# Kernel optimization log

Measured on AMD Instinct MI355X. Metric: run time of the kernel, lower is better.

## Reference

```python
import jax, jax.numpy as jnp
import numpy as np

N_COLS = 4096
N_ROWS = 4096
H = 64          # args.hidden1
S = 2           # per-edge supp feature count (cv_supp/vc_supp dim 0)
S_VO = 2        # vo_supp feature dim
S_CO = 2        # co_supp feature dim
EDGE_DENSITY = 0.03


def setup_inputs() -> dict:
    key = jax.random.key(0)
    ks = jax.random.split(key, 20)
    col_hidden = jax.random.normal(ks[0], (N_COLS, H), jnp.float32)
    row_hidden = jax.random.normal(ks[1], (N_ROWS, H), jnp.float32)
    obj_hidden = jax.random.normal(ks[2], (1, H), jnp.float32)
    # sparse bipartite adjacency encoded in supp[0] != 0 (as in the TF code)
    mask = jax.random.bernoulli(ks[3], EDGE_DENSITY, (N_ROWS, N_COLS))
    cv_supp = jax.random.normal(ks[4], (S, N_ROWS, N_COLS), jnp.float32) * mask[None]
    vc_supp = jnp.transpose(cv_supp, (0, 2, 1))  # [S, ncols, nrows]
    vo_supp = jax.random.normal(ks[5], (N_COLS, S_VO), jnp.float32)
    co_supp = jax.random.normal(ks[6], (N_ROWS, S_CO), jnp.float32)
    w = 0.05
    W_vo = jax.random.normal(ks[7], (2 * H, H), jnp.float32) * w
    W_oc = jax.random.normal(ks[8], (2 * H, H), jnp.float32) * w
    W_vc = jax.random.normal(ks[9], (2 * H, H), jnp.float32) * w
    W_co = jax.random.normal(ks[10], (2 * H, H), jnp.float32) * w
    W_ov = jax.random.normal(ks[11], (2 * H, H), jnp.float32) * w
    W_cv = jax.random.normal(ks[12], (2 * H, H), jnp.float32) * w
    # attention scorer nets: Dense(concat_dim -> 1) + sigmoid
    w_attn_vo = jax.random.normal(ks[13], (2 * H + S_VO, 1), jnp.float32) * 0.1
    b_attn_vo = jnp.zeros((), jnp.float32)
    w_attn_co = jax.random.normal(ks[14], (2 * H + S_CO, 1), jnp.float32) * 0.1
    b_attn_co = jnp.zeros((), jnp.float32)
    # pairwise attn nets decomposed into [col | supp | row] weight slices
    w_cv_col = jax.random.normal(ks[15], (H,), jnp.float32) * 0.1
    w_cv_supp = jax.random.normal(ks[16], (S,), jnp.float32) * 0.1
    w_cv_row = jax.random.normal(ks[17], (H,), jnp.float32) * 0.1
    b_cv = jnp.zeros((), jnp.float32)
    w_vc_row = jax.random.normal(ks[18], (H,), jnp.float32) * 0.1
    w_vc_supp = jax.random.normal(ks[19], (S,), jnp.float32) * 0.1
    w_vc_col = jax.random.normal(jax.random.fold_in(key, 99), (H,), jnp.float32) * 0.1
    b_vc = jnp.zeros((), jnp.float32)
    return dict(col_hidden=col_hidden, row_hidden=row_hidden, obj_hidden=obj_hidden,
                cv_supp=cv_supp, vc_supp=vc_supp, vo_supp=vo_supp, co_supp=co_supp,
                W_vo=W_vo, W_oc=W_oc, W_vc=W_vc, W_co=W_co, W_ov=W_ov, W_cv=W_cv,
                w_attn_vo=w_attn_vo, b_attn_vo=b_attn_vo,
                w_attn_co=w_attn_co, b_attn_co=b_attn_co,
                w_cv_col=w_cv_col, w_cv_supp=w_cv_supp, w_cv_row=w_cv_row, b_cv=b_cv,
                w_vc_row=w_vc_row, w_vc_supp=w_vc_supp, w_vc_col=w_vc_col, b_vc=b_vc)


def _forward(col_hidden, row_hidden, obj_hidden, cv_supp, vc_supp, vo_supp, co_supp,
             W_vo, W_oc, W_vc, W_co, W_ov, W_cv,
             w_attn_vo, b_attn_vo, w_attn_co, b_attn_co,
             w_cv_col, w_cv_supp, w_cv_row, b_cv,
             w_vc_row, w_vc_supp, w_vc_col, b_vc):
    act = jax.nn.relu
    ncols, nrows = col_hidden.shape[0], row_hidden.shape[0]
    # ---- v -> o: attend over all columns, update obj node ----
    vo_in = jnp.concatenate([col_hidden, vo_supp,
                             jnp.broadcast_to(obj_hidden, (ncols, H))], axis=1)
    a_vo = jax.nn.sigmoid(vo_in @ w_attn_vo + b_attn_vo)          # [ncols, 1]
    v_o_out = a_vo.T @ col_hidden                                  # [1, H]
    obj = act(jnp.concatenate([obj_hidden, v_o_out], axis=1) @ W_vo)
    # ---- v -> c: per-row ragged neighbor attention, vectorized via masked pairwise scores ----
    nbr_cv = cv_supp[0] != 0                                       # [nrows, ncols]
    logits_cv = ((row_hidden @ w_cv_row)[:, None]
                 + (col_hidden @ w_cv_col)[None, :]
                 + jnp.einsum('snc,s->nc', cv_supp, w_cv_supp) + b_cv)
    score_cv = jnp.where(nbr_cv, jax.nn.sigmoid(logits_cv), 0.0)   # [nrows, ncols]
    v_out = score_cv @ col_hidden                                  # [nrows, H]
    o_c_out = act(jnp.concatenate([jnp.broadcast_to(obj, (nrows, H)), row_hidden], axis=1) @ W_oc)
    row_next = act(jnp.concatenate([o_c_out, v_out], axis=1) @ W_vc)
    # ---- c -> o ----
    co_in = jnp.concatenate([row_next, co_supp,
                             jnp.broadcast_to(obj, (nrows, H))], axis=1)
    a_co = jax.nn.sigmoid(co_in @ w_attn_co + b_attn_co)           # [nrows, 1]
    c_o_out = a_co.T @ row_next                                    # [1, H]
    obj = act(jnp.concatenate([obj, c_o_out], axis=1) @ W_co)
    # ---- c -> v ----
    nbr_vc = vc_supp[0] != 0                                       # [ncols, nrows]
    logits_vc = ((col_hidden @ w_vc_col)[:, None]
                 + (row_next @ w_vc_row)[None, :]
                 + jnp.einsum('scn,s->cn', vc_supp, w_vc_supp) + b_vc)
    score_vc = jnp.where(nbr_vc, jax.nn.sigmoid(logits_vc), 0.0)   # [ncols, nrows]
    c_out = score_vc @ row_next                                    # [ncols, H]
    o_v_out = act(jnp.concatenate([jnp.broadcast_to(obj, (ncols, H)), col_hidden], axis=1) @ W_ov)
    col_next = act(jnp.concatenate([o_v_out, c_out], axis=1) @ W_cv)
    return col_next, row_next, obj


def reference(col_hidden, row_hidden, obj_hidden, cv_supp, vc_supp, vo_supp, co_supp,
              W_vo, W_oc, W_vc, W_co, W_ov, W_cv,
              w_attn_vo, b_attn_vo, w_attn_co, b_attn_co,
              w_cv_col, w_cv_supp, w_cv_row, b_cv,
              w_vc_row, w_vc_supp, w_vc_col, b_vc):
    col_next, row_next, obj = _forward(
        col_hidden, row_hidden, obj_hidden, cv_supp, vc_supp, vo_supp, co_supp,
        W_vo, W_oc, W_vc, W_co, W_ov, W_cv,
        w_attn_vo, b_attn_vo, w_attn_co, b_attn_co,
        w_cv_col, w_cv_supp, w_cv_row, b_cv,
        w_vc_row, w_vc_supp, w_vc_col, b_vc)
    # original layer also passes the supp tensors through unchanged
    return (col_next, row_next, obj, cv_supp, vc_supp, vo_supp, co_supp)
```

## Files before the change

### kernel.cpp

```cpp
#include <hip/hip_runtime.h>
#include <math.h>

typedef float f4  __attribute__((ext_vector_type(4)));
typedef short s8v __attribute__((ext_vector_type(8)));
typedef unsigned short u16;
typedef u16 us4 __attribute__((ext_vector_type(4)));

#define PLANE (4096*4096)

#define OUT_COL 0
#define OUT_ROW 262144
#define OUT_OBJ 524288
#define OUT_CV  524352
#define OUT_VC  34078784
#define OUT_VO  67633216
#define OUT_CO  67641408

#define WS_VO_P  0
#define WS_CO_P  1024
#define WS_OBJ1  2048
#define WS_RDCV  2112
#define WS_CDCV  6208
#define WS_RDVC  10304
#define WS_CDVC  14400
#define WS_GPART 18496
#define WS_SC    2115648
#define WS_BT1   10504256
#define WS_BT2   10635328

__device__ __forceinline__ float sigf(float x) {
    return 1.0f / (1.0f + __expf(-x));
}
__device__ __forceinline__ u16 f2bf(float x) {
    unsigned u = __float_as_uint(x);
    return (u16)((u + 0x7FFFu + ((u >> 16) & 1u)) >> 16);
}

__device__ __forceinline__ void transpose_tile(int k0, int t,
    const float* __restrict__ X, u16* __restrict__ BT, float* lds )
{
    #pragma unroll
    for (int it = 0; it < 4; ++it) {
        const int idx = it * 256 + t;
        const int r = idx >> 4, c4 = (idx & 15) * 4;
        f4 v = *(const f4*)(X + (size_t)(k0 + r) * 64 + c4);
        *(f4*)(lds + r * 72 + c4) = v;
    }
    __syncthreads();
    #pragma unroll
    for (int it = 0; it < 4; ++it) {
        const int idx = it * 256 + t;
        const int h = idx >> 4, q = (idx & 15) * 4;
        us4 o;
        o.x = f2bf(lds[(q + 0) * 72 + h]);
        o.y = f2bf(lds[(q + 1) * 72 + h]);
        o.z = f2bf(lds[(q + 2) * 72 + h]);
        o.w = f2bf(lds[(q + 3) * 72 + h]);
        *(us4*)(BT + (size_t)h * 4096 + k0 + q) = o;
    }
}

__device__ __forceinline__ void attn_body(
    int blk, int t, const float* __restrict__ X, const float* __restrict__ supp,
    const float* __restrict__ obj, const float* __restrict__ wat,
    const float* __restrict__ bat, float* __restrict__ accP,
    float* sA, float* sAcc)
{
    const int i = blk * 256 + t;
    float od = 0.f;
    for (int h = 0; h < 64; ++h) od += obj[h] * wat[66 + h];
    float x = bat[0] + od + supp[i*2] * wat[64] + supp[i*2+1] * wat[65];
    const f4* Xr = (const f4*)(X + i*64);
    f4 xd = 0.f;
    #pragma unroll
    for (int q = 0; q < 16; ++q) xd += Xr[q] * ((const f4*)wat)[q];
    x += xd.x + xd.y + xd.z + xd.w;
    sA[t] = sigf(x);
    if (t < 64) sAcc[t] = 0.f;
    __syncthreads();
    const int w = t >> 6, h = t & 63;
    const int base = blk * 256 + w * 64;
    float partial = 0.f;
    for (int j = 0; j < 64; ++j)
        partial += sA[w*64 + j] * X[(base + j)*64 + h];
    atomicAdd(&sAcc[h], partial);
    __syncthreads();
    if (t < 64) accP[blk*64 + t] = sAcc[t];
}

__global__ __launch_bounds__(256) void k_front(
    const float* __restrict__ col_hidden, const float* __restrict__ row_hidden,
    const float* __restrict__ w_cv_col, const float* __restrict__ w_vc_col,
    const float* __restrict__ w_cv_row,
    float* __restrict__ cdcv, float* __restrict__ cdvc, float* __restrict__ rdcv,
    const float* __restrict__ vo_supp, const float* __restrict__ co_supp,
    float* __restrict__ out_vo, float* __restrict__ out_co,
    const float* __restrict__ obj_hidden, const float* __restrict__ w_attn_vo,
    const float* __restrict__ b_attn_vo, float* __restrict__ voP,
    u16* __restrict__ BT1)
{
    __shared__ float sA[256];
    __shared__ float sAcc[64];
    __shared__ float tr[64*72];
    const int t = threadIdx.x;
    if (blockIdx.x < 3072) {
        const int gw = blockIdx.x * 4 + (t >> 6);
        const int lane = t & 63;
        const int which = gw >> 12;
        const int row = gw & 4095;
        const float* x; const float* w; float* dst;
        if (which == 0)      { x = col_hidden; w = w_cv_col; dst = cdcv; }
        else if (which == 1) { x = col_hidden; w = w_vc_col; dst = cdvc; }
        else                 { x = row_hidden; w = w_cv_row; dst = rdcv; }
        float v = x[row * 64 + lane] * w[lane];
        #pragma unroll
        for (int off = 32; off; off >>= 1) v += __shfl_down(v, off, 64);
        if (lane == 0) dst[row] = v;
        return;
    }
    if (blockIdx.x < 3088) {
        const int idx = (blockIdx.x - 3072) * 256 + t;
        if (idx < 2048) ((f4*)out_vo)[idx] = ((const f4*)vo_supp)[idx];
        else            ((f4*)out_co)[idx - 2048] = ((const f4*)co_supp)[idx - 2048];
        return;
    }
    if (blockIdx.x < 3104) {
        attn_body(blockIdx.x - 3088, t, col_hidden, vo_supp, obj_hidden,
                  w_attn_vo, b_attn_vo, voP, sA, sAcc);
        return;
    }
    transpose_tile((blockIdx.x - 3104) * 64, t, col_hidden, BT1, tr);
}

__global__ __launch_bounds__(256) void k_attn(
    const float* __restrict__ X, const float* __restrict__ supp,
    const float* __restrict__ obj, const float* __restrict__ wat,
    const float* __restrict__ bat, float* __restrict__ accP,
    u16* __restrict__ BT2)
{
    __shared__ float sA[256];
    __shared__ float sAcc[64];
    __shared__ float tr[64*72];
    if (blockIdx.x < 16) {
        attn_body(blockIdx.x, threadIdx.x, X, supp, obj, wat, bat, accP, sA, sAcc);
        return;
    }
    transpose_tile((blockIdx.x - 16) * 64, threadIdx.x, X, BT2, tr);
}

__global__ __launch_bounds__(256) void k_copy(
    const float* __restrict__ a, const float* __restrict__ b,
    float* __restrict__ da, float* __restrict__ db)
{
    const int t = threadIdx.x;
    const f4* src; f4* dst; size_t off;
    if (blockIdx.x < 8192) { src = (const f4*)a; dst = (f4*)da; off = (size_t)blockIdx.x * 1024; }
    else                   { src = (const f4*)b; dst = (f4*)db; off = (size_t)(blockIdx.x - 8192) * 1024; }
    #pragma unroll
    for (int it = 0; it < 4; ++it) {
        const size_t i = off + t + it * 256;
        dst[i] = src[i];
    }
}

__global__ __launch_bounds__(256) void k_score(
    const float* __restrict__ supp0, const float* __restrict__ supp1,
    const float* __restrict__ perrow, const float* __restrict__ percol,
    const float* __restrict__ wsup, const float* __restrict__ bias,
    u16* __restrict__ score)
{
    const float w0 = wsup[0], w1 = wsup[1], bv = bias[0];
    const float rd = perrow[blockIdx.x];
    const size_t base = (size_t)blockIdx.x * 1024 + threadIdx.x;
    #pragma unroll
    for (int it = 0; it < 4; ++it) {
        const size_t idx = base + it * 256;
        const int j0 = (int)(idx & 1023) * 4;
        f4 a0 = ((const f4*)supp0)[idx];
        f4 a1 = ((const f4*)supp1)[idx];
        f4 cd = *(const f4*)(percol + j0);
        f4 lg = rd + cd + w0 * a0 + w1 * a1 + bv;
        us4 o;
        o.x = (a0.x != 0.f) ? f2bf(sigf(lg.x)) : (u16)0;
        o.y = (a0.y != 0.f) ? f2bf(sigf(lg.y)) : (u16)0;
        o.z = (a0.z != 0.f) ? f2bf(sigf(lg.z)) : (u16)0;
        o.w = (a0.w != 0.f) ? f2bf(sigf(lg.w)) : (u16)0;
        ((us4*)score)[idx] = o;
    }
}

__global__ __launch_bounds__(256, 4) void k_gemm(
    const u16* __restrict__ sc, const u16* __restrict__ BT,
    float* __restrict__ part,
    const float* __restrict__ objL, const float* __restrict__ objRp,
    const float* __restrict__ Wobj, float* __restrict__ objDst)
{
    __shared__ float rsum[64];
    const int t = threadIdx.x;
    if (blockIdx.x == 512) {
        if (t < 64) {
            float r = 0.f;
            for (int b = 0; b < 16; ++b) r += objRp[b*64 + t];
            rsum[t] = r;
        }
        __syncthreads();
        if (t < 64) {
            float acc = 0.f;
            for (int k = 0; k < 64; ++k) acc += objL[k] * Wobj[k*64 + t];
            for (int k = 0; k < 64; ++k) acc += rsum[k] * Wobj[(64+k)*64 + t];
            objDst[t] = fmaxf(acc, 0.f);
        }
        return;
    }
    const int mblk = blockIdx.x >> 3;
    const int ks   = blockIdx.x & 7;
    const int wv   = t >> 6, lane = t & 63;
    const int i0   = mblk * 64 + wv * 16;
    const int m    = lane & 15, quad = lane >> 4;
    const int k0   = ks * 512;

    f4 acc0 = 0.f, acc1 = 0.f, acc2 = 0.f, acc3 = 0.f;
    const u16* ap  = sc + (size_t)(i0 + m) * 4096 + k0 + quad * 8;
    const u16* bp  = BT + (size_t)m * 4096 + k0 + quad * 8;
    #pragma unroll 4
    for (int kc = 0; kc < 512; kc += 32) {
        s8v a  = *(const s8v*)(ap + kc);
        s8v b0 = *(const s8v*)(bp + kc);
        s8v b1 = *(const s8v*)(bp + 16 * 4096 + kc);
        s8v b2 = *(const s8v*)(bp + 32 * 4096 + kc);
        s8v b3 = *(const s8v*)(bp + 48 * 4096 + kc);
        acc0 = __builtin_amdgcn_mfma_f32_16x16x32_bf16(a, b0, acc0, 0, 0, 0);
        acc1 = __builtin_amdgcn_mfma_f32_16x16x32_bf16(a, b1, acc1, 0, 0, 0);
        acc2 = __builtin_amdgcn_mfma_f32_16x16x32_bf16(a, b2, acc2, 0, 0, 0);
        acc3 = __builtin_amdgcn_mfma_f32_16x16x32_bf16(a, b3, acc3, 0, 0, 0);
    }
    float* pb = part + (size_t)ks * 262144;
    #pragma unroll
    for (int r = 0; r < 4; ++r) {
        const size_t ro = (size_t)(i0 + quad * 4 + r) * 64 + m;
        pb[ro +  0] = acc0[r];
        pb[ro + 16] = acc1[r];
        pb[ro + 32] = acc2[r];
        pb[ro + 48] = acc3[r];
    }
}

__global__ __launch_bounds__(256) void k_mlp2(
    const float* __restrict__ objx, const float* __restrict__ base,
    const float* __restrict__ W1, const float* __restrict__ part,
    const float* __restrict__ W2, float* __restrict__ dst,
    const float* __restrict__ wvcrow, float* __restrict__ rdvc)
{
    __shared__ float mid[4][64];
    __shared__ float accs[4][64];
    const int t = threadIdx.x, w = t >> 6, h = t & 63;
    const int n = blockIdx.x * 4 + w;
    float v = 0.f;
    #pragma unroll
    for (int j = 0; j < 8; ++j) v += part[(size_t)j * 262144 + n*64 + h];
    accs[w][h] = v;
    float m = 0.f;
    for (int k = 0; k < 64; ++k) m += objx[k] * W1[k*64 + h];
    for (int k = 0; k < 64; ++k) m += base[n*64 + k] * W1[(64+k)*64 + h];
    mid[w][h] = fmaxf(m, 0.f);
    __syncthreads();
    float o = 0.f;
    for (int k = 0; k < 64; ++k) o += mid[w][k] * W2[k*64 + h];
    for (int k = 0; k < 64; ++k) o += accs[w][k] * W2[(64+k)*64 + h];
    o = fmaxf(o, 0.f);
    dst[n*64 + h] = o;
    if (rdvc) {
        float rv = o * wvcrow[h];
        #pragma unroll
        for (int off = 32; off; off >>= 1) rv += __shfl_down(rv, off, 64);
        if (h == 0) rdvc[n] = rv;
    }
}

extern "C" void kernel_launch(void* const* d_in, const int* in_sizes, int n_in,
                              void* d_out, int out_size, void* d_ws, size_t ws_size,
                              hipStream_t stream)
{
    const float* col_hidden = (const float*)d_in[0];
    const float* row_hidden = (const float*)d_in[1];
    const float* obj_hidden = (const float*)d_in[2];
    const float* cv_supp    = (const float*)d_in[3];
    const float* vc_supp    = (const float*)d_in[4];
    const float* vo_supp    = (const float*)d_in[5];
    const float* co_supp    = (const float*)d_in[6];
    const float* W_vo       = (const float*)d_in[7];
    const float* W_oc       = (const float*)d_in[8];
    const float* W_vc       = (const float*)d_in[9];
    const float* W_co       = (const float*)d_in[10];
    const float* W_ov       = (const float*)d_in[11];
    const float* W_cv       = (const float*)d_in[12];
    const float* w_attn_vo  = (const float*)d_in[13];
    const float* b_attn_vo  = (const float*)d_in[14];
    const float* w_attn_co  = (const float*)d_in[15];
    const float* b_attn_co  = (const float*)d_in[16];
    const float* w_cv_col   = (const float*)d_in[17];
    const float* w_cv_supp  = (const float*)d_in[18];
    const float* w_cv_row   = (const float*)d_in[19];
    const float* b_cv       = (const float*)d_in[20];
    const float* w_vc_row   = (const float*)d_in[21];
    const float* w_vc_supp  = (const float*)d_in[22];
    const float* w_vc_col   = (const float*)d_in[23];
    const float* b_vc       = (const float*)d_in[24];

    float* out = (float*)d_out;
    float* ws  = (float*)d_ws;
    u16* SC  = (u16*)(ws + WS_SC);
    u16* BT1 = (u16*)(ws + WS_BT1);
    u16* BT2 = (u16*)(ws + WS_BT2);

    k_front<<<3168, 256, 0, stream>>>(col_hidden, row_hidden, w_cv_col, w_vc_col, w_cv_row,
                                      ws + WS_CDCV, ws + WS_CDVC, ws + WS_RDCV,
                                      vo_supp, co_supp, out + OUT_VO, out + OUT_CO,
                                      obj_hidden, w_attn_vo, b_attn_vo, ws + WS_VO_P, BT1);
    k_copy<<<16384, 256, 0, stream>>>(cv_supp, vc_supp, out + OUT_CV, out + OUT_VC);
    k_score<<<4096, 256, 0, stream>>>(cv_supp, cv_supp + PLANE,
                                      ws + WS_RDCV, ws + WS_CDCV, w_cv_supp, b_cv, SC);
    k_gemm<<<513, 256, 0, stream>>>(SC, BT1, ws + WS_GPART,
                                    obj_hidden, ws + WS_VO_P, W_vo, ws + WS_OBJ1);
    k_mlp2<<<1024, 256, 0, stream>>>(ws + WS_OBJ1, row_hidden, W_oc, ws + WS_GPART, W_vc,
                                     out + OUT_ROW, w_vc_row, ws + WS_RDVC);
    k_attn<<<80, 256, 0, stream>>>(out + OUT_ROW, co_supp, ws + WS_OBJ1, w_attn_co,
                                   b_attn_co, ws + WS_CO_P, BT2);
    k_score<<<4096, 256, 0, stream>>>(vc_supp, vc_supp + PLANE,
                                      ws + WS_CDVC, ws + WS_RDVC, w_vc_supp, b_vc, SC);
    k_gemm<<<513, 256, 0, stream>>>(SC, BT2, ws + WS_GPART,
                                    ws + WS_OBJ1, ws + WS_CO_P, W_co, out + OUT_OBJ);
    k_mlp2<<<1024, 256, 0, stream>>>(out + OUT_OBJ, col_hidden, W_ov, ws + WS_GPART, W_cv,
                                     out + OUT_COL, nullptr, nullptr);
}
```

Baseline: 647.1 us.

## Fuse score computation and supp passthrough copy into the bf16 MFMA GEMM

Result: faster. 578.5 us (-10.6%).

```diff
diff --git a/kernel.cpp b/kernel.cpp
--- a/kernel.cpp
+++ b/kernel.cpp
@@ -24,9 +24,8 @@
 #define WS_RDVC  10304
 #define WS_CDVC  14400
 #define WS_GPART 18496
-#define WS_SC    2115648
-#define WS_BT1   10504256
-#define WS_BT2   10635328
+#define WS_BT1   4212800
+#define WS_BT2   4343872
 
 __device__ __forceinline__ float sigf(float x) {
     return 1.0f / (1.0f + __expf(-x));
@@ -148,56 +147,19 @@
     transpose_tile((blockIdx.x - 16) * 64, threadIdx.x, X, BT2, tr);
 }
 
-__global__ __launch_bounds__(256) void k_copy(
-    const float* __restrict__ a, const float* __restrict__ b,
-    float* __restrict__ da, float* __restrict__ db)
-{
-    const int t = threadIdx.x;
-    const f4* src; f4* dst; size_t off;
-    if (blockIdx.x < 8192) { src = (const f4*)a; dst = (f4*)da; off = (size_t)blockIdx.x * 1024; }
-    else                   { src = (const f4*)b; dst = (f4*)db; off = (size_t)(blockIdx.x - 8192) * 1024; }
-    #pragma unroll
-    for (int it = 0; it < 4; ++it) {
-        const size_t i = off + t + it * 256;
-        dst[i] = src[i];
-    }
-}
-
-__global__ __launch_bounds__(256) void k_score(
+__global__ __launch_bounds__(256, 4) void k_fgemm(
     const float* __restrict__ supp0, const float* __restrict__ supp1,
-    const float* __restrict__ perrow, const float* __restrict__ percol,
+    const u16* __restrict__ BT,
+    const float* __restrict__ rdot, const float* __restrict__ cdot,
     const float* __restrict__ wsup, const float* __restrict__ bias,
-    u16* __restrict__ score)
-{
-    const float w0 = wsup[0], w1 = wsup[1], bv = bias[0];
-    const float rd = perrow[blockIdx.x];
-    const size_t base = (size_t)blockIdx.x * 1024 + threadIdx.x;
-    #pragma unroll
-    for (int it = 0; it < 4; ++it) {
-        const size_t idx = base + it * 256;
-        const int j0 = (int)(idx & 1023) * 4;
-        f4 a0 = ((const f4*)supp0)[idx];
-        f4 a1 = ((const f4*)supp1)[idx];
-        f4 cd = *(const f4*)(percol + j0);
-        f4 lg = rd + cd + w0 * a0 + w1 * a1 + bv;
-        us4 o;
-        o.x = (a0.x != 0.f) ? f2bf(sigf(lg.x)) : (u16)0;
-        o.y = (a0.y != 0.f) ? f2bf(sigf(lg.y)) : (u16)0;
-        o.z = (a0.z != 0.f) ? f2bf(sigf(lg.z)) : (u16)0;
-        o.w = (a0.w != 0.f) ? f2bf(sigf(lg.w)) : (u16)0;
-        ((us4*)score)[idx] = o;
-    }
-}
-
-__global__ __launch_bounds__(256, 4) void k_gemm(
-    const u16* __restrict__ sc, const u16* __restrict__ BT,
+    float* __restrict__ pass0, float* __restrict__ pass1,
     float* __restrict__ part,
     const float* __restrict__ objL, const float* __restrict__ objRp,
     const float* __restrict__ Wobj, float* __restrict__ objDst)
 {
     __shared__ float rsum[64];
     const int t = threadIdx.x;
-    if (blockIdx.x == 512) {
+    if (blockIdx.x == 1024) {
         if (t < 64) {
             float r = 0.f;
             for (int b = 0; b < 16; ++b) r += objRp[b*64 + t];
@@ -212,19 +174,42 @@
         }
         return;
     }
-    const int mblk = blockIdx.x >> 3;
-    const int ks   = blockIdx.x & 7;
+    const int mblk = blockIdx.x >> 4;
+    const int ks   = blockIdx.x & 15;
     const int wv   = t >> 6, lane = t & 63;
     const int i0   = mblk * 64 + wv * 16;
     const int m    = lane & 15, quad = lane >> 4;
-    const int k0   = ks * 512;
+    const int k0   = ks * 256;
+    const float rd = rdot[i0 + m];
+    const float w0 = wsup[0], w1 = wsup[1], bv = bias[0];
 
     f4 acc0 = 0.f, acc1 = 0.f, acc2 = 0.f, acc3 = 0.f;
-    const u16* ap  = sc + (size_t)(i0 + m) * 4096 + k0 + quad * 8;
-    const u16* bp  = BT + (size_t)m * 4096 + k0 + quad * 8;
-    #pragma unroll 4
-    for (int kc = 0; kc < 512; kc += 32) {
-        s8v a  = *(const s8v*)(ap + kc);
+    const size_t arow = (size_t)(i0 + m) * 4096 + k0 + quad * 8;
+    const u16* bp = BT + (size_t)m * 4096 + k0 + quad * 8;
+
+    for (int kc = 0; kc < 256; kc += 32) {
+        f4 a0l = *(const f4*)(supp0 + arow + kc);
+        f4 a0h = *(const f4*)(supp0 + arow + kc + 4);
+        f4 a1l = *(const f4*)(supp1 + arow + kc);
+        f4 a1h = *(const f4*)(supp1 + arow + kc + 4);
+        *(f4*)(pass0 + arow + kc)     = a0l;
+        *(f4*)(pass0 + arow + kc + 4) = a0h;
+        *(f4*)(pass1 + arow + kc)     = a1l;
+        *(f4*)(pass1 + arow + kc + 4) = a1h;
+        const int kabs = k0 + quad * 8 + kc;
+        f4 cdl = *(const f4*)(cdot + kabs);
+        f4 cdh = *(const f4*)(cdot + kabs + 4);
+        f4 lgl = rd + cdl + w0 * a0l + w1 * a1l + bv;
+        f4 lgh = rd + cdh + w0 * a0h + w1 * a1h + bv;
+        s8v a;
+        a[0] = (short)((a0l.x != 0.f) ? f2bf(sigf(lgl.x)) : (u16)0);
+        a[1] = (short)((a0l.y != 0.f) ? f2bf(sigf(lgl.y)) : (u16)0);
+        a[2] = (short)((a0l.z != 0.f) ? f2bf(sigf(lgl.z)) : (u16)0);
+        a[3] = (short)((a0l.w != 0.f) ? f2bf(sigf(lgl.w)) : (u16)0);
+        a[4] = (short)((a0h.x != 0.f) ? f2bf(sigf(lgh.x)) : (u16)0);
+        a[5] = (short)((a0h.y != 0.f) ? f2bf(sigf(lgh.y)) : (u16)0);
+        a[6] = (short)((a0h.z != 0.f) ? f2bf(sigf(lgh.z)) : (u16)0);
+        a[7] = (short)((a0h.w != 0.f) ? f2bf(sigf(lgh.w)) : (u16)0);
         s8v b0 = *(const s8v*)(bp + kc);
         s8v b1 = *(const s8v*)(bp + 16 * 4096 + kc);
         s8v b2 = *(const s8v*)(bp + 32 * 4096 + kc);
@@ -257,7 +242,7 @@
     const int n = blockIdx.x * 4 + w;
     float v = 0.f;
     #pragma unroll
-    for (int j = 0; j < 8; ++j) v += part[(size_t)j * 262144 + n*64 + h];
+    for (int j = 0; j < 16; ++j) v += part[(size_t)j * 262144 + n*64 + h];
     accs[w][h] = v;
     float m = 0.f;
     for (int k = 0; k < 64; ++k) m += objx[k] * W1[k*64 + h];
@@ -309,7 +294,6 @@
 
     float* out = (float*)d_out;
     float* ws  = (float*)d_ws;
-    u16* SC  = (u16*)(ws + WS_SC);
     u16* BT1 = (u16*)(ws + WS_BT1);
     u16* BT2 = (u16*)(ws + WS_BT2);
 
@@ -317,19 +301,18 @@
                                       ws + WS_CDCV, ws + WS_CDVC, ws + WS_RDCV,
                                       vo_supp, co_supp, out + OUT_VO, out + OUT_CO,
                                       obj_hidden, w_attn_vo, b_attn_vo, ws + WS_VO_P, BT1);
-    k_copy<<<16384, 256, 0, stream>>>(cv_supp, vc_supp, out + OUT_CV, out + OUT_VC);
-    k_score<<<4096, 256, 0, stream>>>(cv_supp, cv_supp + PLANE,
-                                      ws + WS_RDCV, ws + WS_CDCV, w_cv_supp, b_cv, SC);
-    k_gemm<<<513, 256, 0, stream>>>(SC, BT1, ws + WS_GPART,
-                                    obj_hidden, ws + WS_VO_P, W_vo, ws + WS_OBJ1);
+    k_fgemm<<<1025, 256, 0, stream>>>(cv_supp, cv_supp + PLANE, BT1,
+                                      ws + WS_RDCV, ws + WS_CDCV, w_cv_supp, b_cv,
+                                      out + OUT_CV, out + OUT_CV + PLANE, ws + WS_GPART,
+                                      obj_hidden, ws + WS_VO_P, W_vo, ws + WS_OBJ1);
     k_mlp2<<<1024, 256, 0, stream>>>(ws + WS_OBJ1, row_hidden, W_oc, ws + WS_GPART, W_vc,
                                      out + OUT_ROW, w_vc_row, ws + WS_RDVC);
     k_attn<<<80, 256, 0, stream>>>(out + OUT_ROW, co_supp, ws + WS_OBJ1, w_attn_co,
                                    b_attn_co, ws + WS_CO_P, BT2);
-    k_score<<<4096, 256, 0, stream>>>(vc_supp, vc_supp + PLANE,
-                                      ws + WS_CDVC, ws + WS_RDVC, w_vc_supp, b_vc, SC);
-    k_gemm<<<513, 256, 0, stream>>>(SC, BT2, ws + WS_GPART,
-                                    ws + WS_OBJ1, ws + WS_CO_P, W_co, out + OUT_OBJ);
+    k_fgemm<<<1025, 256, 0, stream>>>(vc_supp, vc_supp + PLANE, BT2,
+                                      ws + WS_CDVC, ws + WS_RDVC, w_vc_supp, b_vc,
+                                      out + OUT_VC, out + OUT_VC + PLANE, ws + WS_GPART,
+                                      ws + WS_OBJ1, ws + WS_CO_P, W_co, out + OUT_OBJ);
     k_mlp2<<<1024, 256, 0, stream>>>(out + OUT_OBJ, col_hidden, W_ov, ws + WS_GPART, W_cv,
                                      out + OUT_COL, nullptr, nullptr);
 }
```
